# Kernel tuning notes

Measured on AMD Instinct MI355X. Metric: run time of the kernel, lower is better.

## Reference

```python
import jax, jax.numpy as jnp
import numpy as np

B, L, D = 4, 4096, 1024
C = 8.0  # fixed exponent scale from the module (self.c = 8)


def setup_inputs() -> dict:
    key = jax.random.key(0)
    ks = jax.random.split(key, 4)
    std = 1.0 / np.sqrt(D)  # kaiming normal, fan_in, linear
    x = jax.random.normal(ks[0], (B, L, D), dtype=jnp.float32)
    Wa = jax.random.normal(ks[1], (D, D), dtype=jnp.float32) * std
    Wx = jax.random.normal(ks[2], (D, D), dtype=jnp.float32) * std
    ba = jnp.zeros((D,), dtype=jnp.float32)
    bx = jnp.zeros((D,), dtype=jnp.float32)
    # lmbd ~ U(0.9, 0.999)
    lmbd = 0.9 + 0.099 * jax.random.uniform(ks[3], (D,), dtype=jnp.float32)
    return {"x": x, "Wa": Wa, "Wx": Wx, "ba": ba, "bx": bx, "lmbd": lmbd}


def reference(x, Wa, Wx, ba, bx, lmbd):
    # a = sigmoid(lmbd) computed once at init in the original module
    log_a = jnp.log(jax.nn.sigmoid(lmbd))  # [D], negative
    # Batched projections upfront (F.linear uses W @ x^T, i.e. x @ W.T)
    r = jax.nn.sigmoid(jnp.einsum('bld,hd->blh', x, Wa) + ba)  # recurrence gate
    i = jax.nn.sigmoid(jnp.einsum('bld,hd->blh', x, Wx) + bx)  # input gate
    a_t = jnp.exp(C * r * log_a)                 # a ** (c * r), [B,L,D]
    b_t = jnp.sqrt(1.0 - a_t * a_t) * (i * x)    # [B,L,D]
    # Linear recurrence h_t = a_t * h_{t-1} + b_t, h_0 = 0
    def step(h, ab):
        at, bt = ab
        h = at * h + bt
        return h, h
    h0 = jnp.zeros((x.shape[0], x.shape[2]), dtype=x.dtype)
    _, y = jax.lax.scan(step, h0, (jnp.swapaxes(a_t, 0, 1), jnp.swapaxes(b_t, 0, 1)))
    return jnp.swapaxes(y, 0, 1)  # [B, L, D]
```

## Files before the change

### kernel.cpp

```cpp
#include <hip/hip_runtime.h>
#include <stdint.h>
#include <math.h>


#define D_DIM 1024
#define L_DIM 4096
#define B_DIM 4
#define M_DIM (B_DIM * L_DIM)
#define N_DIM (2 * D_DIM)
#define K_DIM D_DIM
#define NC 32
#define CL (L_DIM / NC)
#define L2E 1.4426950408889634f

typedef __attribute__((ext_vector_type(8))) short short8;
typedef __attribute__((ext_vector_type(4))) short short4v;
typedef __attribute__((ext_vector_type(4))) float float4v;

__device__ __forceinline__ unsigned short f2bf(float f) {
  unsigned u = __float_as_uint(f);
  u += 0x7fffu + ((u >> 16) & 1u);
  return (unsigned short)(u >> 16);
}
__device__ __forceinline__ float bf2f(unsigned short h) {
  return __uint_as_float((unsigned)h << 16);
}
__device__ __forceinline__ short f2h(float f) {
  _Float16 h = (_Float16)f;
  return __builtin_bit_cast(short, h);
}

#define NX16 (M_DIM * K_DIM / 8)
#define NW16 (N_DIM * K_DIM / 8)

__global__ void pack_all(const float* __restrict__ x, const float* __restrict__ Wa,
                         const float* __restrict__ Wx, short* __restrict__ Xs,
                         short* __restrict__ Ws) {
  int t = blockIdx.x * 256 + threadIdx.x;
  const float* src;
  short8* dst;
  int u;
  if (t < NX16) {
    u = t; src = x; dst = (short8*)Xs;
  } else {
    u = t - NX16;
    if (u >= NW16) return;
    dst = (short8*)Ws;
    int row = ((u >> 11) << 4) | (u & 15);
    src = (row < D_DIM) ? Wa : (Wx - (size_t)D_DIM * K_DIM);
  }
  int r  = u & 15;
  int kc = (u >> 4) & 3;
  int k0 = (u >> 6) & 31;
  int R  = u >> 11;
  int m = R * 16 + r;
  int k = (k0 * 4 + kc) * 8;
  const float4v* s4 = (const float4v*)(src + (size_t)m * 1024 + k);
  float4v v0 = s4[0], v1 = s4[1];
  short8 o;
  o[0] = (short)f2bf(v0.x); o[1] = (short)f2bf(v0.y);
  o[2] = (short)f2bf(v0.z); o[3] = (short)f2bf(v0.w);
  o[4] = (short)f2bf(v1.x); o[5] = (short)f2bf(v1.y);
  o[6] = (short)f2bf(v1.z); o[7] = (short)f2bf(v1.w);
  dst[u] = o;
}

__global__ __launch_bounds__(256, 4) void gemm_gates(
    const short* __restrict__ Xs,
    const short* __restrict__ Ws,
    const float* __restrict__ xf,
    const float* __restrict__ ba,
    const float* __restrict__ bx,
    const float* __restrict__ lmbd,
    short* __restrict__ e_out,
    unsigned short* __restrict__ g_out)
{
  __shared__ __align__(16) char smem[17664];

  const int bid = blockIdx.y * 16 + blockIdx.x;
  const int nb  = (bid & 7) * 256 + (bid >> 3);
  const int tile_n = (nb & 15) * 128;
  const int tile_m = (nb >> 4) * 128;
  const int tid  = threadIdx.x;
  const int wave = tid >> 6;
  const int lane = tid & 63;
  const int row16 = lane & 15;
  const int quad  = lane >> 4;
  const int wave_m = (wave & 1) * 64;
  const int wave_n = (wave >> 1) * 64;

  short* As = (short*)smem;
  short* Bs = (short*)(smem + 8192);
  char* AsB = smem;
  char* BsB = smem + 8192;

  float4v acc[4][4] = {};

  for (int kk = 0; kk < 32; ++kk) {
#pragma unroll
    for (int p = 0; p < 2; ++p) {
      const int G = p * 4 + wave;
      const size_t RgA = (size_t)((tile_m >> 4) + G);
      const size_t RgB = (size_t)((tile_n >> 4) + G);
      __builtin_amdgcn_global_load_lds(
          (const __attribute__((address_space(1))) void*)(Xs + ((RgA * 32 + kk) * 64 + lane) * 8),
          (__attribute__((address_space(3))) void*)(AsB + G * 1024),
          16, 0, 0);
      __builtin_amdgcn_global_load_lds(
          (const __attribute__((address_space(1))) void*)(Ws + ((RgB * 32 + kk) * 64 + lane) * 8),
          (__attribute__((address_space(3))) void*)(BsB + G * 1024),
          16, 0, 0);
    }
    __syncthreads();

    short8 af[4], bfr[4];
#pragma unroll
    for (int i = 0; i < 4; ++i)
      af[i] = *(const short8*)&As[((wave & 1) * 4 + i) * 512 + lane * 8];
#pragma unroll
    for (int i = 0; i < 4; ++i)
      bfr[i] = *(const short8*)&Bs[((wave >> 1) * 4 + i) * 512 + lane * 8];

#pragma unroll
    for (int mi = 0; mi < 4; ++mi)
#pragma unroll
      for (int ni = 0; ni < 4; ++ni)
        acc[mi][ni] = __builtin_amdgcn_mfma_f32_16x16x32_bf16(af[mi], bfr[ni], acc[mi][ni], 0, 0, 0);
    __syncthreads();
  }

  float* Ts = (float*)smem + (size_t)wave * (16 * 68);
  const int colg = (lane & 15) * 4;
  const int rrow = lane >> 4;
  const bool is_a = (tile_n < D_DIM);
  const int ch0 = (is_a ? tile_n : tile_n - D_DIM) + wave_n + colg;

  float4v bias4, la84;
  if (is_a) {
    bias4 = *(const float4v*)(ba + ch0);
    float4v lm4 = *(const float4v*)(lmbd + ch0);
#pragma unroll
    for (int k = 0; k < 4; ++k)
      la84[k] = -8.0f * __builtin_amdgcn_logf(1.0f + __builtin_amdgcn_exp2f(-lm4[k] * L2E));
  } else {
    bias4 = *(const float4v*)(bx + ch0);
  }

#pragma unroll
  for (int mi = 0; mi < 4; ++mi) {
#pragma unroll
    for (int ni = 0; ni < 4; ++ni)
#pragma unroll
      for (int r = 0; r < 4; ++r)
        Ts[(quad * 4 + r) * 68 + ni * 16 + row16] = acc[mi][ni][r];
#pragma unroll
    for (int j = 0; j < 4; ++j) {
      int lr = j * 4 + rrow;
      float4v z = *(const float4v*)&Ts[lr * 68 + colg];
      size_t gm = (size_t)(tile_m + wave_m + mi * 16 + lr);
      short4v o;
      if (is_a) {
#pragma unroll
        for (int k = 0; k < 4; ++k) {
          float s = __builtin_amdgcn_rcpf(1.0f + __builtin_amdgcn_exp2f(-(z[k] + bias4[k]) * L2E));
          o[k] = f2h(s * la84[k]);
        }
        *(short4v*)(e_out + gm * D_DIM + ch0) = o;
      } else {
        float4v xv = *(const float4v*)(xf + gm * D_DIM + ch0);
#pragma unroll
        for (int k = 0; k < 4; ++k) {
          float s = __builtin_amdgcn_rcpf(1.0f + __builtin_amdgcn_exp2f(-(z[k] + bias4[k]) * L2E));
          o[k] = (short)f2bf(s * xv[k]);
        }
        *(short4v*)((short*)g_out + gm * D_DIM + ch0) = o;
      }
    }
  }
}

__global__ void scan_phase1(const short* __restrict__ e, const unsigned short* __restrict__ g,
                            float* __restrict__ P, float* __restrict__ Q) {
  int d = blockIdx.x * 256 + threadIdx.x;
  int c = blockIdx.y;
  int b = blockIdx.z;
  const size_t base = ((size_t)(b * L_DIM + c * CL)) * D_DIM + d;
  float Pv = 1.0f, Qv = 0.0f;
#pragma unroll 4
  for (int t = 0; t < CL; ++t) {
    float ev = (float)__builtin_bit_cast(_Float16, e[base + (size_t)t * D_DIM]);
    float at = __builtin_amdgcn_exp2f(ev);
    float gv = bf2f(g[base + (size_t)t * D_DIM]);
    float bt = sqrtf(fmaxf(1.0f - at * at, 0.0f)) * gv;
    Qv = fmaf(at, Qv, bt);
    Pv *= at;
  }
  int idx = (b * NC + c) * D_DIM + d;
  P[idx] = Pv;
  Q[idx] = Qv;
}

__global__ void scan_phase3(const short* __restrict__ e, const unsigned short* __restrict__ g,
                            const float* __restrict__ P, const float* __restrict__ Q,
                            float* __restrict__ y) {
  int d = blockIdx.x * 256 + threadIdx.x;
  int c = blockIdx.y;
  int b = blockIdx.z;
  float h = 0.0f;
#pragma unroll 4
  for (int cc = 0; cc < c; ++cc) {
    int idx = (b * NC + cc) * D_DIM + d;
    h = fmaf(P[idx], h, Q[idx]);
  }
  const size_t base = ((size_t)(b * L_DIM + c * CL)) * D_DIM + d;
#pragma unroll 4
  for (int t = 0; t < CL; ++t) {
    float ev = (float)__builtin_bit_cast(_Float16, e[base + (size_t)t * D_DIM]);
    float at = __builtin_amdgcn_exp2f(ev);
    float gv = bf2f(g[base + (size_t)t * D_DIM]);
    float bt = sqrtf(fmaxf(1.0f - at * at, 0.0f)) * gv;
    h = fmaf(at, h, bt);
    y[base + (size_t)t * D_DIM] = h;
  }
}

extern "C" void kernel_launch(void* const* d_in, const int* in_sizes, int n_in,
                              void* d_out, int out_size, void* d_ws, size_t ws_size,
                              hipStream_t stream) {
  const float* x    = (const float*)d_in[0];
  const float* Wa   = (const float*)d_in[1];
  const float* Wx   = (const float*)d_in[2];
  const float* ba   = (const float*)d_in[3];
  const float* bx   = (const float*)d_in[4];
  const float* lmbd = (const float*)d_in[5];
  float* y = (float*)d_out;

  char* ws = (char*)d_ws;
  short* Xs             = (short*)ws;
  short* Wsz            = (short*)(ws + 33554432);
  short* e_buf          = (short*)(ws + 37748736);
  unsigned short* g_buf = (unsigned short*)(ws + 71303168);
  float* P              = (float*)(ws + 104857600);
  float* Q              = (float*)(ws + 105381888);

  pack_all<<<(NX16 + NW16) / 256, 256, 0, stream>>>(x, Wa, Wx, Xs, Wsz);

  dim3 gg(N_DIM / 128, M_DIM / 128);
  gemm_gates<<<gg, 256, 0, stream>>>(Xs, Wsz, x, ba, bx, lmbd, e_buf, g_buf);

  dim3 sg(D_DIM / 256, NC, B_DIM);
  scan_phase1<<<sg, 256, 0, stream>>>(e_buf, g_buf, P, Q);
  scan_phase3<<<sg, 256, 0, stream>>>(e_buf, g_buf, P, Q, y);
}
```

Measured before the change: 246.5 us.

## Stage scan chunks into LDS with async global loads and double chunk count

The scan kernels now bulk-load each chunk's e and g slices into shared memory through global_load_lds before running the sequential recurrence. This replaces the dependent per-timestep 2-byte global loads. The chunk count doubles from 32 to 64, so each chunk is 64 steps and there are twice as many blocks. In phase 3 the carry-in prefix over P/Q overlaps with the staging loads. Costs are 64KB of LDS per block, which limits occupancy, and a longer serial prefix over previous chunks in phase 3. The Q buffer offset moves to fit the larger P.

```diff
diff --git a/kernel.cpp b/kernel.cpp
--- a/kernel.cpp
+++ b/kernel.cpp
@@ -9,7 +9,7 @@
 #define M_DIM (B_DIM * L_DIM)
 #define N_DIM (2 * D_DIM)
 #define K_DIM D_DIM
-#define NC 32
+#define NC 64
 #define CL (L_DIM / NC)
 #define L2E 1.4426950408889634f
 
@@ -179,48 +179,87 @@
   }
 }
 
-__global__ void scan_phase1(const short* __restrict__ e, const unsigned short* __restrict__ g,
-                            float* __restrict__ P, float* __restrict__ Q) {
-  int d = blockIdx.x * 256 + threadIdx.x;
-  int c = blockIdx.y;
-  int b = blockIdx.z;
-  const size_t base = ((size_t)(b * L_DIM + c * CL)) * D_DIM + d;
+
+__device__ __forceinline__ void stage_slice(const char* gsrc, char* ldst,
+                                            size_t rowBytes, int tid) {
+#pragma unroll
+  for (int i = 0; i < 8; ++i) {
+    int gIdx = i * 256 + tid;
+    int t = gIdx >> 5;
+    int c16 = gIdx & 31;
+    const char* src = gsrc + (size_t)t * (D_DIM * 2) + c16 * 16;
+    __builtin_amdgcn_global_load_lds(
+        (const __attribute__((address_space(1))) void*)src,
+        (__attribute__((address_space(3))) void*)(ldst + i * 4096 + (tid & 192) * 16),
+        16, 0, 0);
+  }
+  (void)rowBytes;
+}
+
+__global__ __launch_bounds__(256) void scan_phase1(
+    const short* __restrict__ e, const unsigned short* __restrict__ g,
+    float* __restrict__ P, float* __restrict__ Q) {
+  __shared__ __align__(16) char lds[65536];
+  const int tid = threadIdx.x;
+  const int dg = blockIdx.x;
+  const int c  = blockIdx.y;
+  const int b  = blockIdx.z;
+  const size_t rowBase = ((size_t)(b * L_DIM + c * CL)) * D_DIM + dg * 256;
+
+  stage_slice((const char*)(e + rowBase), lds, 512, tid);
+  stage_slice((const char*)(g + rowBase), lds + 32768, 512, tid);
+  __syncthreads();
+
+  const short* eL = (const short*)lds;
+  const unsigned short* gL = (const unsigned short*)(lds + 32768);
   float Pv = 1.0f, Qv = 0.0f;
-#pragma unroll 4
+#pragma unroll 8
   for (int t = 0; t < CL; ++t) {
-    float ev = (float)__builtin_bit_cast(_Float16, e[base + (size_t)t * D_DIM]);
+    float ev = (float)__builtin_bit_cast(_Float16, eL[t * 256 + tid]);
     float at = __builtin_amdgcn_exp2f(ev);
-    float gv = bf2f(g[base + (size_t)t * D_DIM]);
+    float gv = bf2f(gL[t * 256 + tid]);
     float bt = sqrtf(fmaxf(1.0f - at * at, 0.0f)) * gv;
     Qv = fmaf(at, Qv, bt);
     Pv *= at;
   }
-  int idx = (b * NC + c) * D_DIM + d;
+  const int idx = (b * NC + c) * D_DIM + dg * 256 + tid;
   P[idx] = Pv;
   Q[idx] = Qv;
 }
 
-__global__ void scan_phase3(const short* __restrict__ e, const unsigned short* __restrict__ g,
-                            const float* __restrict__ P, const float* __restrict__ Q,
-                            float* __restrict__ y) {
-  int d = blockIdx.x * 256 + threadIdx.x;
-  int c = blockIdx.y;
-  int b = blockIdx.z;
+__global__ __launch_bounds__(256) void scan_phase3(
+    const short* __restrict__ e, const unsigned short* __restrict__ g,
+    const float* __restrict__ P, const float* __restrict__ Q,
+    float* __restrict__ y) {
+  __shared__ __align__(16) char lds[65536];
+  const int tid = threadIdx.x;
+  const int dg = blockIdx.x;
+  const int c  = blockIdx.y;
+  const int b  = blockIdx.z;
+  const size_t rowBase = ((size_t)(b * L_DIM + c * CL)) * D_DIM + dg * 256;
+
+  stage_slice((const char*)(e + rowBase), lds, 512, tid);
+  stage_slice((const char*)(g + rowBase), lds + 32768, 512, tid);
+
   float h = 0.0f;
-#pragma unroll 4
+  const int dcol = dg * 256 + tid;
   for (int cc = 0; cc < c; ++cc) {
-    int idx = (b * NC + cc) * D_DIM + d;
+    const int idx = (b * NC + cc) * D_DIM + dcol;
     h = fmaf(P[idx], h, Q[idx]);
   }
-  const size_t base = ((size_t)(b * L_DIM + c * CL)) * D_DIM + d;
-#pragma unroll 4
+  __syncthreads();
+
+  const short* eL = (const short*)lds;
+  const unsigned short* gL = (const unsigned short*)(lds + 32768);
+  float* yrow = y + rowBase + tid;
+#pragma unroll 8
   for (int t = 0; t < CL; ++t) {
-    float ev = (float)__builtin_bit_cast(_Float16, e[base + (size_t)t * D_DIM]);
+    float ev = (float)__builtin_bit_cast(_Float16, eL[t * 256 + tid]);
     float at = __builtin_amdgcn_exp2f(ev);
-    float gv = bf2f(g[base + (size_t)t * D_DIM]);
+    float gv = bf2f(gL[t * 256 + tid]);
     float bt = sqrtf(fmaxf(1.0f - at * at, 0.0f)) * gv;
     h = fmaf(at, h, bt);
-    y[base + (size_t)t * D_DIM] = h;
+    yrow[(size_t)t * D_DIM] = h;
   }
 }
 
@@ -241,7 +280,7 @@
   short* e_buf          = (short*)(ws + 37748736);
   unsigned short* g_buf = (unsigned short*)(ws + 71303168);
   float* P              = (float*)(ws + 104857600);
-  float* Q              = (float*)(ws + 105381888);
+  float* Q              = (float*)(ws + 105906176);
 
   pack_all<<<(NX16 + NW16) / 256, 256, 0, stream>>>(x, Wa, Wx, Xs, Wsz);
 
```

Result: slower. 264.4 us (+7.3%).
